# Kernel optimization log

Measured on AMD Instinct MI355X. Metric: run time of the kernel, lower is better.

Reference implementation:

```python
import jax, jax.numpy as jnp
import numpy as np
from jax import lax

WINDOW_SIZE = 11
SIGMA = 1.5
C1 = 0.01 ** 2
C2 = 0.03 ** 2


def _gaussian_window(channels: int) -> jnp.ndarray:
    x = np.arange(WINDOW_SIZE)
    g = np.exp(-((x - WINDOW_SIZE // 2) ** 2) / (2.0 * SIGMA ** 2))
    g = g / g.sum()
    w2d = np.outer(g, g).astype(np.float32)  # [k,k]
    # depthwise kernel: [C, 1, k, k] in OIHW with feature_group_count=C
    return jnp.asarray(np.tile(w2d[None, None], (channels, 1, 1, 1)))


def _depthwise_blur(x: jnp.ndarray, window: jnp.ndarray) -> jnp.ndarray:
    pad = WINDOW_SIZE // 2
    return lax.conv_general_dilated(
        x, window,
        window_strides=(1, 1),
        padding=[(pad, pad), (pad, pad)],
        feature_group_count=x.shape[1],
        dimension_numbers=("NCHW", "OIHW", "NCHW"),
    )


def setup_inputs() -> dict:
    key = jax.random.key(0)
    k1, k2 = jax.random.split(key)
    pred = jax.random.normal(k1, (16, 3, 512, 512), dtype=jnp.float32)
    target = jax.random.normal(k2, (16, 3, 512, 512), dtype=jnp.float32)
    return {"pred": pred, "target": target}


def reference(pred, target):
    pred = (pred + 1.0) / 2.0
    target = (target + 1.0) / 2.0
    channels = pred.shape[1]
    window = _gaussian_window(channels)

    mu_p = _depthwise_blur(pred, window)
    mu_t = _depthwise_blur(target, window)
    mu_p_sq = mu_p * mu_p
    mu_t_sq = mu_t * mu_t
    mu_pt = mu_p * mu_t

    sigma_p_sq = _depthwise_blur(pred * pred, window) - mu_p_sq
    sigma_t_sq = _depthwise_blur(target * target, window) - mu_t_sq
    sigma_pt = _depthwise_blur(pred * target, window) - mu_pt

    ssim_map = ((2.0 * mu_pt + C1) * (2.0 * sigma_pt + C2)) / (
        (mu_p_sq + mu_t_sq + C1) * (sigma_p_sq + sigma_t_sq + C2)
    )
    return 1.0 - jnp.mean(ssim_map)
```

## Files before the change

### kernel.cpp

```cpp
#include <hip/hip_runtime.h>
#include <math.h>


#define IMG   512
#define TW    64
#define TH    16
#define HALO  5
#define IW    74
#define IWP   76
#define NRG   4
#define NSLOT (IW * NRG)
#define GXD   8
#define GYD   32
#define GZD   48
#define NB    (GXD * GYD * GZD)
#define C1c   0.0001f
#define C2c   0.0009f
#define NTOTAL 12582912.0f

struct GaussW { float g[11]; };

template <bool USE_ATOMIC>
__global__ __launch_bounds__(256, 6) void ssim_main(
    const float* __restrict__ pred,
    const float* __restrict__ target,
    float* __restrict__ sink,
    GaussW gw)
{
    __shared__ __align__(16) float hb[5][TH][IWP];
    __shared__ float red[4];

    const int tid = threadIdx.x;
    const int tx0 = blockIdx.x * TW;
    const int ty0 = blockIdx.y * TH;
    const float* __restrict__ pbase = pred   + (size_t)blockIdx.z * (IMG*IMG);
    const float* __restrict__ tbase = target + (size_t)blockIdx.z * (IMG*IMG);

    const bool interior = (blockIdx.x >= 1) & (blockIdx.x <= GXD - 2) &
                          (blockIdx.y >= 1) & (blockIdx.y <= GYD - 2);

    for (int slot = tid; slot < NSLOT; slot += 256) {
        const int rg = slot / IW;
        const int c  = slot - rg * IW;
        const int gx = tx0 - HALO + c;
        const int gy0 = ty0 + rg * 4 - HALO;

        float pv[14], tv[14];
        if (interior) {
            const float* pp = pbase + (size_t)gy0 * IMG + gx;
            const float* tp = tbase + (size_t)gy0 * IMG + gx;
            #pragma unroll
            for (int k = 0; k < 14; ++k) {
                pv[k] = pp[k * IMG];
                tv[k] = tp[k * IMG];
            }
        } else {
            const bool xin = (gx >= 0) & (gx < IMG);
            #pragma unroll
            for (int k = 0; k < 14; ++k) {
                int gy = gy0 + k;
                bool in = xin & (gy >= 0) & (gy < IMG);
                int idx = in ? (gy * IMG + gx) : 0;
                float p = pbase[idx];
                float t = tbase[idx];
                pv[k] = in ? p : 0.0f;
                tv[k] = in ? t : 0.0f;
            }
        }

        float acc[5][4];
        #pragma unroll
        for (int ch = 0; ch < 5; ++ch)
            #pragma unroll
            for (int j = 0; j < 4; ++j) acc[ch][j] = 0.0f;

        #pragma unroll
        for (int k = 0; k < 14; ++k) {
            float ps = fmaf(pv[k], 0.5f, 0.5f);
            float ts = fmaf(tv[k], 0.5f, 0.5f);
            float v2 = ps * ps;
            float v3 = ts * ts;
            float v4 = ps * ts;
            #pragma unroll
            for (int j = 0; j < 4; ++j) {
                const int kk = k - j;
                if (kk >= 0 && kk < 11) {
                    float w = gw.g[kk];
                    acc[0][j] = fmaf(w, ps, acc[0][j]);
                    acc[1][j] = fmaf(w, ts, acc[1][j]);
                    acc[2][j] = fmaf(w, v2, acc[2][j]);
                    acc[3][j] = fmaf(w, v3, acc[3][j]);
                    acc[4][j] = fmaf(w, v4, acc[4][j]);
                }
            }
        }
        #pragma unroll
        for (int ch = 0; ch < 5; ++ch)
            #pragma unroll
            for (int j = 0; j < 4; ++j)
                hb[ch][rg * 4 + j][c] = acc[ch][j];
    }
    __syncthreads();

    const int r  = tid >> 4;
    const int c4 = (tid & 15) * 4;

    float res[5][4];
    #pragma unroll
    for (int ch = 0; ch < 5; ++ch) {
        const float* row = &hb[ch][r][c4];
        float x[16];
        #pragma unroll
        for (int q = 0; q < 4; ++q) {
            float4 v = ((const float4*)row)[q];
            x[4*q+0] = v.x; x[4*q+1] = v.y; x[4*q+2] = v.z; x[4*q+3] = v.w;
        }
        float a0 = 0.f, a1 = 0.f, a2 = 0.f, a3 = 0.f;
        #pragma unroll
        for (int k = 0; k < 11; ++k) {
            float w = gw.g[k];
            a0 = fmaf(w, x[k + 0], a0);
            a1 = fmaf(w, x[k + 1], a1);
            a2 = fmaf(w, x[k + 2], a2);
            a3 = fmaf(w, x[k + 3], a3);
        }
        res[ch][0] = a0; res[ch][1] = a1; res[ch][2] = a2; res[ch][3] = a3;
    }

    float lsum = 0.0f;
    #pragma unroll
    for (int j = 0; j < 4; ++j) {
        float mp = res[0][j], mt = res[1][j];
        float mp2 = mp * mp, mt2 = mt * mt, mpt = mp * mt;
        float sig_p  = res[2][j] - mp2;
        float sig_t  = res[3][j] - mt2;
        float sig_pt = res[4][j] - mpt;
        float num = (2.0f * mpt + C1c) * (2.0f * sig_pt + C2c);
        float den = (mp2 + mt2 + C1c) * (sig_p + sig_t + C2c);
        lsum += num / den;
    }

    #pragma unroll
    for (int off = 32; off > 0; off >>= 1)
        lsum += __shfl_down(lsum, off, 64);
    if ((tid & 63) == 0) red[tid >> 6] = lsum;
    __syncthreads();
    if (tid == 0) {
        float s = red[0] + red[1] + red[2] + red[3];
        if (USE_ATOMIC) {
            atomicAdd(sink, s);
        } else {
            int bid = blockIdx.x + GXD * (blockIdx.y + GYD * blockIdx.z);
            sink[bid] = s;
        }
    }
}

__global__ __launch_bounds__(256) void ssim_reduce(const float* __restrict__ partials,
                                                   float* __restrict__ out)
{
    __shared__ float red[4];
    const int tid = threadIdx.x;
    float s = 0.0f;
    const float4* p4 = (const float4*)partials;
    #pragma unroll
    for (int j = 0; j < NB / 1024; ++j) {
        float4 v = p4[tid + 256 * j];
        s += v.x + v.y + v.z + v.w;
    }
    #pragma unroll
    for (int off = 32; off > 0; off >>= 1)
        s += __shfl_down(s, off, 64);
    if ((tid & 63) == 0) red[tid >> 6] = s;
    __syncthreads();
    if (tid == 0)
        out[0] = 1.0f - (red[0] + red[1] + red[2] + red[3]) / NTOTAL;
}

__global__ void ssim_zero(float* accum) { accum[0] = 0.0f; }
__global__ void ssim_final(const float* accum, float* out) {
    out[0] = 1.0f - accum[0] / NTOTAL;
}

extern "C" void kernel_launch(void* const* d_in, const int* in_sizes, int n_in,
                              void* d_out, int out_size, void* d_ws, size_t ws_size,
                              hipStream_t stream) {
    const float* pred   = (const float*)d_in[0];
    const float* target = (const float*)d_in[1];
    float* out = (float*)d_out;

    GaussW gw;
    double vals[11], s = 0.0;
    for (int i = 0; i < 11; ++i) {
        double d = (double)i - 5.0;
        vals[i] = exp(-(d * d) / (2.0 * 1.5 * 1.5));
        s += vals[i];
    }
    for (int i = 0; i < 11; ++i) gw.g[i] = (float)(vals[i] / s);

    dim3 grid(GXD, GYD, GZD);
    if (ws_size >= (size_t)NB * sizeof(float)) {
        float* partials = (float*)d_ws;
        ssim_main<false><<<grid, 256, 0, stream>>>(pred, target, partials, gw);
        ssim_reduce<<<1, 256, 0, stream>>>(partials, out);
    } else {
        float* accum = (float*)d_ws;
        ssim_zero<<<1, 1, 0, stream>>>(accum);
        ssim_main<true><<<grid, 256, 0, stream>>>(pred, target, accum, gw);
        ssim_final<<<1, 1, 0, stream>>>(accum, out);
    }
}
```

Baseline: 167.4 us.

## Compute separable Gaussian blur as bf16 MFMA banded-matrix products

Replaces the scalar fp32 FMA vertical and horizontal blur passes with MFMA 16x16x32 bf16 matrix multiplies against a banded Gaussian weight matrix held in shared memory. Inputs, squares, cross products and the intermediate vertical results are rounded to bf16, which also halves the shared-memory footprint. The aim is to move the convolution arithmetic, which dominates the kernel, onto the matrix units. In exchange, bf16 rounding feeding E[x^2]-mu^2 invites cancellation error that could push the result outside tolerance. The work split is also uneven: 5 column chunks across 4 waves, and 16-wide row loads coalesce less well.

```diff
diff --git a/kernel.cpp b/kernel.cpp
--- a/kernel.cpp
+++ b/kernel.cpp
@@ -1,140 +1,140 @@
 #include <hip/hip_runtime.h>
+#include <hip/hip_bf16.h>
 #include <math.h>
 
 
-#define IMG   512
-#define TW    64
-#define TH    16
-#define HALO  5
-#define IW    74
-#define IWP   76
-#define NRG   4
-#define NSLOT (IW * NRG)
-#define GXD   8
-#define GYD   32
-#define GZD   48
-#define NB    (GXD * GYD * GZD)
-#define C1c   0.0001f
-#define C2c   0.0009f
+#define IMG 512
+#define TW 64
+#define TH 16
+#define GXD 8
+#define GYD 32
+#define GZD 48
+#define NB (GXD * GYD * GZD)
+#define VBS 88
+#define C1c 0.0001f
+#define C2c 0.0009f
 #define NTOTAL 12582912.0f
 
+typedef short bf16x8 __attribute__((ext_vector_type(8)));
+typedef float f32x4 __attribute__((ext_vector_type(4)));
+
 struct GaussW { float g[11]; };
 
+__device__ __forceinline__ unsigned int f2bf2(float a, float b) {
+    union { __hip_bfloat162 h; unsigned int u; } cv;
+    cv.h = __float22bfloat162_rn(make_float2(a, b));
+    return cv.u;
+}
+
 template <bool USE_ATOMIC>
-__global__ __launch_bounds__(256, 6) void ssim_main(
+__global__ __launch_bounds__(256, 4) void ssim_main(
     const float* __restrict__ pred,
     const float* __restrict__ target,
     float* __restrict__ sink,
     GaussW gw)
 {
-    __shared__ __align__(16) float hb[5][TH][IWP];
+    __shared__ unsigned short Wmat[16][32];
+    __shared__ unsigned short vb[5][16][VBS];
     __shared__ float red[4];
 
-    const int tid = threadIdx.x;
-    const int tx0 = blockIdx.x * TW;
-    const int ty0 = blockIdx.y * TH;
-    const float* __restrict__ pbase = pred   + (size_t)blockIdx.z * (IMG*IMG);
-    const float* __restrict__ tbase = target + (size_t)blockIdx.z * (IMG*IMG);
+    const int tid  = threadIdx.x;
+    const int w    = tid >> 6;
+    const int lane = tid & 63;
+    const int quad = lane >> 4;
+    const int n16  = lane & 15;
+    const int tx0  = blockIdx.x * TW;
+    const int ty0  = blockIdx.y * TH;
+    const float* __restrict__ pbase = pred   + (size_t)blockIdx.z * (IMG * IMG);
+    const float* __restrict__ tbase = target + (size_t)blockIdx.z * (IMG * IMG);
+
+    for (int idx = tid; idx < 512; idx += 256) {
+        int i = idx >> 5, k = idx & 31, d = k - i;
+        float v = (d >= 0 && d <= 10) ? gw.g[d] : 0.0f;
+        Wmat[i][k] = (unsigned short)(f2bf2(v, 0.0f) & 0xFFFFu);
+    }
+    __syncthreads();
+
+    const bf16x8 wfrag = *(const bf16x8*)&Wmat[n16][quad * 8];
 
     const bool interior = (blockIdx.x >= 1) & (blockIdx.x <= GXD - 2) &
                           (blockIdx.y >= 1) & (blockIdx.y <= GYD - 2);
-
-    for (int slot = tid; slot < NSLOT; slot += 256) {
-        const int rg = slot / IW;
-        const int c  = slot - rg * IW;
-        const int gx = tx0 - HALO + c;
-        const int gy0 = ty0 + rg * 4 - HALO;
-
-        float pv[14], tv[14];
+    const f32x4 z = {0.0f, 0.0f, 0.0f, 0.0f};
+
+    for (int vc = w; vc < 5; vc += 4) {
+        const int gx = tx0 - 5 + 16 * vc + n16;
+        const int k0 = quad * 8;
+        float pv[8], tv[8];
         if (interior) {
-            const float* pp = pbase + (size_t)gy0 * IMG + gx;
-            const float* tp = tbase + (size_t)gy0 * IMG + gx;
+            const float* pp = pbase + (size_t)(ty0 - 5 + k0) * IMG + gx;
+            const float* tp = tbase + (size_t)(ty0 - 5 + k0) * IMG + gx;
             #pragma unroll
-            for (int k = 0; k < 14; ++k) {
-                pv[k] = pp[k * IMG];
-                tv[k] = tp[k * IMG];
+            for (int j = 0; j < 8; ++j) {
+                pv[j] = pp[j * IMG];
+                tv[j] = tp[j * IMG];
             }
         } else {
-            const bool xin = (gx >= 0) & (gx < IMG);
+            const bool xin = (unsigned)gx < (unsigned)IMG;
             #pragma unroll
-            for (int k = 0; k < 14; ++k) {
-                int gy = gy0 + k;
-                bool in = xin & (gy >= 0) & (gy < IMG);
+            for (int j = 0; j < 8; ++j) {
+                int gy = ty0 - 5 + k0 + j;
+                bool in = xin && ((unsigned)gy < (unsigned)IMG);
                 int idx = in ? (gy * IMG + gx) : 0;
-                float p = pbase[idx];
-                float t = tbase[idx];
-                pv[k] = in ? p : 0.0f;
-                tv[k] = in ? t : 0.0f;
+                float a = pbase[idx];
+                float b = tbase[idx];
+                pv[j] = in ? a : 0.0f;
+                tv[j] = in ? b : 0.0f;
             }
         }
-
-        float acc[5][4];
+        union { bf16x8 v; unsigned int u[4]; } fP, fT, fPP, fTT, fPT;
         #pragma unroll
-        for (int ch = 0; ch < 5; ++ch)
-            #pragma unroll
-            for (int j = 0; j < 4; ++j) acc[ch][j] = 0.0f;
-
-        #pragma unroll
-        for (int k = 0; k < 14; ++k) {
-            float ps = fmaf(pv[k], 0.5f, 0.5f);
-            float ts = fmaf(tv[k], 0.5f, 0.5f);
-            float v2 = ps * ps;
-            float v3 = ts * ts;
-            float v4 = ps * ts;
-            #pragma unroll
-            for (int j = 0; j < 4; ++j) {
-                const int kk = k - j;
-                if (kk >= 0 && kk < 11) {
-                    float w = gw.g[kk];
-                    acc[0][j] = fmaf(w, ps, acc[0][j]);
-                    acc[1][j] = fmaf(w, ts, acc[1][j]);
-                    acc[2][j] = fmaf(w, v2, acc[2][j]);
-                    acc[3][j] = fmaf(w, v3, acc[3][j]);
-                    acc[4][j] = fmaf(w, v4, acc[4][j]);
-                }
-            }
-        }
-        #pragma unroll
-        for (int ch = 0; ch < 5; ++ch)
-            #pragma unroll
-            for (int j = 0; j < 4; ++j)
-                hb[ch][rg * 4 + j][c] = acc[ch][j];
-    }
-    __syncthreads();
-
-    const int r  = tid >> 4;
-    const int c4 = (tid & 15) * 4;
-
-    float res[5][4];
+        for (int h = 0; h < 4; ++h) {
+            float p0 = fmaf(pv[2*h],   0.5f, 0.5f);
+            float p1 = fmaf(pv[2*h+1], 0.5f, 0.5f);
+            float t0 = fmaf(tv[2*h],   0.5f, 0.5f);
+            float t1 = fmaf(tv[2*h+1], 0.5f, 0.5f);
+            fP.u[h]  = f2bf2(p0, p1);
+            fT.u[h]  = f2bf2(t0, t1);
+            fPP.u[h] = f2bf2(p0 * p0, p1 * p1);
+            fTT.u[h] = f2bf2(t0 * t0, t1 * t1);
+            fPT.u[h] = f2bf2(p0 * t0, p1 * t1);
+        }
+        f32x4 d0 = __builtin_amdgcn_mfma_f32_16x16x32_bf16(fP.v,  wfrag, z, 0, 0, 0);
+        f32x4 d1 = __builtin_amdgcn_mfma_f32_16x16x32_bf16(fT.v,  wfrag, z, 0, 0, 0);
+        f32x4 d2 = __builtin_amdgcn_mfma_f32_16x16x32_bf16(fPP.v, wfrag, z, 0, 0, 0);
+        f32x4 d3 = __builtin_amdgcn_mfma_f32_16x16x32_bf16(fTT.v, wfrag, z, 0, 0, 0);
+        f32x4 d4 = __builtin_amdgcn_mfma_f32_16x16x32_bf16(fPT.v, wfrag, z, 0, 0, 0);
+        const int vcol = 16 * vc + 4 * quad;
+        {
+            union { ushort4 s; unsigned int u[2]; } pk;
+            pk.u[0] = f2bf2(d0[0], d0[1]); pk.u[1] = f2bf2(d0[2], d0[3]);
+            *(ushort4*)&vb[0][n16][vcol] = pk.s;
+            pk.u[0] = f2bf2(d1[0], d1[1]); pk.u[1] = f2bf2(d1[2], d1[3]);
+            *(ushort4*)&vb[1][n16][vcol] = pk.s;
+            pk.u[0] = f2bf2(d2[0], d2[1]); pk.u[1] = f2bf2(d2[2], d2[3]);
+            *(ushort4*)&vb[2][n16][vcol] = pk.s;
+            pk.u[0] = f2bf2(d3[0], d3[1]); pk.u[1] = f2bf2(d3[2], d3[3]);
+            *(ushort4*)&vb[3][n16][vcol] = pk.s;
+            pk.u[0] = f2bf2(d4[0], d4[1]); pk.u[1] = f2bf2(d4[2], d4[3]);
+            *(ushort4*)&vb[4][n16][vcol] = pk.s;
+        }
+    }
+    __syncthreads();
+
+    f32x4 r[5];
     #pragma unroll
     for (int ch = 0; ch < 5; ++ch) {
-        const float* row = &hb[ch][r][c4];
-        float x[16];
-        #pragma unroll
-        for (int q = 0; q < 4; ++q) {
-            float4 v = ((const float4*)row)[q];
-            x[4*q+0] = v.x; x[4*q+1] = v.y; x[4*q+2] = v.z; x[4*q+3] = v.w;
-        }
-        float a0 = 0.f, a1 = 0.f, a2 = 0.f, a3 = 0.f;
-        #pragma unroll
-        for (int k = 0; k < 11; ++k) {
-            float w = gw.g[k];
-            a0 = fmaf(w, x[k + 0], a0);
-            a1 = fmaf(w, x[k + 1], a1);
-            a2 = fmaf(w, x[k + 2], a2);
-            a3 = fmaf(w, x[k + 3], a3);
-        }
-        res[ch][0] = a0; res[ch][1] = a1; res[ch][2] = a2; res[ch][3] = a3;
+        bf16x8 a = *(const bf16x8*)&vb[ch][n16][16 * w + 8 * quad];
+        r[ch] = __builtin_amdgcn_mfma_f32_16x16x32_bf16(a, wfrag, z, 0, 0, 0);
     }
 
     float lsum = 0.0f;
     #pragma unroll
     for (int j = 0; j < 4; ++j) {
-        float mp = res[0][j], mt = res[1][j];
+        float mp = r[0][j], mt = r[1][j];
         float mp2 = mp * mp, mt2 = mt * mt, mpt = mp * mt;
-        float sig_p  = res[2][j] - mp2;
-        float sig_t  = res[3][j] - mt2;
-        float sig_pt = res[4][j] - mpt;
+        float sig_p  = r[2][j] - mp2;
+        float sig_t  = r[3][j] - mt2;
+        float sig_pt = r[4][j] - mpt;
         float num = (2.0f * mpt + C1c) * (2.0f * sig_pt + C2c);
         float den = (mp2 + mt2 + C1c) * (sig_p + sig_t + C2c);
         lsum += num / den;
@@ -143,7 +143,7 @@
     #pragma unroll
     for (int off = 32; off > 0; off >>= 1)
         lsum += __shfl_down(lsum, off, 64);
-    if ((tid & 63) == 0) red[tid >> 6] = lsum;
+    if (lane == 0) red[w] = lsum;
     __syncthreads();
     if (tid == 0) {
         float s = red[0] + red[1] + red[2] + red[3];
```

Measured after the change: 141.4 us. -15.5%, faster.
